# Kernel tuning notes

Hardware: AMD Instinct MI355X
Metric: run time of the kernel (lower is better)

Reference implementation:

```python
import jax, jax.numpy as jnp
import numpy as np

N = 100000      # nodes
E = 1000000     # edges (before self-loops)
IN_DIM = 256
H = 4           # heads
C = 32          # out_dim per head
NEG_SLOPE = 0.2  # PyG GATConv default negative_slope


def setup_inputs() -> dict:
    key = jax.random.key(0)
    ks = jax.random.split(key, 6)
    x = jax.random.normal(ks[0], (N, IN_DIM), jnp.float32)
    W = jax.random.normal(ks[1], (IN_DIM, H * C), jnp.float32) * (1.0 / np.sqrt(IN_DIM))
    a_src = jax.random.normal(ks[2], (H, C), jnp.float32) * 0.1
    a_dst = jax.random.normal(ks[3], (H, C), jnp.float32) * 0.1
    bias = jnp.zeros((H * C,), jnp.float32)
    edge_index = jax.random.randint(ks[4], (2, E), 0, N, dtype=jnp.int32)
    return {"x": x, "W": W, "a_src": a_src, "a_dst": a_dst, "bias": bias,
            "edge_index": edge_index}


def reference(x, W, a_src, a_dst, bias, edge_index):
    n = x.shape[0]
    # PyG GATConv default: add self-loops
    loops = jnp.arange(n, dtype=edge_index.dtype)
    src = jnp.concatenate([edge_index[0], loops])  # [E+N]
    dst = jnp.concatenate([edge_index[1], loops])  # [E+N]
    # linear transform -> [N, H, C]
    h = (x @ W).reshape(n, H, C)
    # per-node attention logits
    alpha_s = jnp.einsum('nhc,hc->nh', h, a_src)  # [N, H]
    alpha_d = jnp.einsum('nhc,hc->nh', h, a_dst)  # [N, H]
    # per-edge score, LeakyReLU
    e = jax.nn.leaky_relu(alpha_s[src] + alpha_d[dst], NEG_SLOPE)  # [E+N, H]
    # segment softmax over incoming edges of each destination node
    m = jax.lax.stop_gradient(jax.ops.segment_max(e, dst, num_segments=n))
    p = jnp.exp(e - m[dst])
    s = jax.ops.segment_sum(p, dst, num_segments=n)
    alpha = p / (s[dst] + 1e-16)  # [E+N, H]
    # weighted scatter-add of source features
    out = jax.ops.segment_sum(alpha[:, :, None] * h[src], dst, num_segments=n)  # [N, H, C]
    out = out.reshape(n, H * C) + bias
    return jnp.tanh(out)
```

## Files before the change

### kernel.cpp

```cpp
#include <hip/hip_runtime.h>

#define IN_DIM 256
#define HC     128
#define NHEAD  4
#define NEG    0.2f
#define CAP    256
#define AS     264
#define BKT    1024
#define NBMAX  128
#define EPT    16
#define BE     4096

typedef __attribute__((ext_vector_type(8))) short short8v;
typedef __attribute__((ext_vector_type(4))) float f32x4;
typedef __attribute__((ext_vector_type(4))) unsigned short ushort4v;

__device__ __forceinline__ unsigned short bf16_rn(float f) {
    unsigned u = __builtin_bit_cast(unsigned, f);
    return (unsigned short)((u + 0x7fffu + ((u >> 16) & 1u)) >> 16);
}
__device__ __forceinline__ float bf16_to_f32(unsigned short b) {
    unsigned u = ((unsigned)b) << 16;
    return __builtin_bit_cast(float, u);
}
__device__ __forceinline__ float fast_tanh(float x) {
    float t = __expf(2.f * x);
    return fmaf(-2.f, __builtin_amdgcn_rcpf(t + 1.f), 1.f);
}

__global__ void pack_w_kernel(const float* __restrict__ W,
                              unsigned short* __restrict__ w_hi) {
    int t = blockIdx.x * 256 + threadIdx.x;
    if (t >= 8 * 8 * 64) return;
    int l  = t & 63;
    int ct = (t >> 6) & 7;
    int s  = t >> 9;
    int kbase = s * 32 + (l >> 4) * 8;
    int col   = ct * 16 + (l & 15);
    size_t base = (size_t)t * 8;
#pragma unroll
    for (int e = 0; e < 8; ++e)
        w_hi[base + e] = bf16_rn(W[(size_t)(kbase + e) * HC + col]);
}

__global__ __launch_bounds__(512) void gemm_mfma_kernel(const float* __restrict__ x,
                                                        const unsigned short* __restrict__ w_hi,
                                                        const float* __restrict__ a_src,
                                                        const float* __restrict__ a_dst,
                                                        unsigned short* __restrict__ h_bf,
                                                        float* __restrict__ alpha_s,
                                                        float* __restrict__ alpha_d, int n) {
    __shared__ unsigned short s_hi[64][AS];
    __shared__ unsigned short s_lo[64][AS];
    __shared__ float pS[64][4];
    __shared__ float pD[64][4];

    const int tid = threadIdx.x;
    const int l   = tid & 63;
    const int wv  = tid >> 6;
    const int row0 = blockIdx.x * 64;

    const float4* x4 = reinterpret_cast<const float4*>(x);
#pragma unroll
    for (int i = 0; i < 8; ++i) {
        int f = tid + i * 512;
        int row = f >> 6, c4 = f & 63;
        float4 v = make_float4(0.f, 0.f, 0.f, 0.f);
        if (row0 + row < n) v = x4[(size_t)(row0 + row) * 64 + c4];
        float e[4] = {v.x, v.y, v.z, v.w};
        ushort4v hi, lo;
#pragma unroll
        for (int q = 0; q < 4; ++q) {
            unsigned short h16 = bf16_rn(e[q]);
            hi[q] = h16;
            lo[q] = bf16_rn(e[q] - bf16_to_f32(h16));
        }
        *reinterpret_cast<ushort4v*>(&s_hi[row][c4 * 4]) = hi;
        *reinterpret_cast<ushort4v*>(&s_lo[row][c4 * 4]) = lo;
    }
    __syncthreads();

    const int ct_g = wv & 3;
    const int rt_g = wv >> 2;
    const int rrow = l & 15;
    const int koff = (l >> 4) * 8;

    f32x4 acc[2][2];
#pragma unroll
    for (int a = 0; a < 2; ++a)
#pragma unroll
        for (int b = 0; b < 2; ++b) acc[a][b] = (f32x4){0.f, 0.f, 0.f, 0.f};

    for (int s = 0; s < 8; ++s) {
        short8v bh[2];
#pragma unroll
        for (int c = 0; c < 2; ++c) {
            int ct = ct_g * 2 + c;
            bh[c] = *reinterpret_cast<const short8v*>(w_hi + ((size_t)(s * 8 + ct) * 64 + l) * 8);
        }
#pragma unroll
        for (int r = 0; r < 2; ++r) {
            int arow = rt_g * 32 + r * 16 + rrow;
            short8v ah = *reinterpret_cast<const short8v*>(&s_hi[arow][koff + s * 32]);
            short8v al = *reinterpret_cast<const short8v*>(&s_lo[arow][koff + s * 32]);
#pragma unroll
            for (int c = 0; c < 2; ++c) {
                acc[r][c] = __builtin_amdgcn_mfma_f32_16x16x32_bf16(ah, bh[c], acc[r][c], 0, 0, 0);
                acc[r][c] = __builtin_amdgcn_mfma_f32_16x16x32_bf16(al, bh[c], acc[r][c], 0, 0, 0);
            }
        }
    }

#pragma unroll
    for (int r = 0; r < 2; ++r) {
#pragma unroll
        for (int c = 0; c < 2; ++c) {
            int col = (ct_g * 2 + c) * 16 + (l & 15);
#pragma unroll
            for (int q = 0; q < 4; ++q) {
                int row = row0 + rt_g * 32 + r * 16 + (l >> 4) * 4 + q;
                if (row < n) h_bf[(size_t)row * HC + col] = bf16_rn(acc[r][c][q]);
            }
        }
    }

    float asc[2], adc[2];
#pragma unroll
    for (int c = 0; c < 2; ++c) {
        int col = (ct_g * 2 + c) * 16 + (l & 15);
        asc[c] = a_src[col];
        adc[c] = a_dst[col];
    }
#pragma unroll
    for (int r = 0; r < 2; ++r) {
#pragma unroll
        for (int q = 0; q < 4; ++q) {
            float vS = acc[r][0][q] * asc[0] + acc[r][1][q] * asc[1];
            float vD = acc[r][0][q] * adc[0] + acc[r][1][q] * adc[1];
#pragma unroll
            for (int m = 1; m < 16; m <<= 1) {
                vS += __shfl_xor(vS, m);
                vD += __shfl_xor(vD, m);
            }
            if ((l & 15) == 0) {
                int rl = rt_g * 32 + r * 16 + (l >> 4) * 4 + q;
                pS[rl][ct_g] = vS;
                pD[rl][ct_g] = vD;
            }
        }
    }
    __syncthreads();
    if (tid < 256) {
        int rl = tid >> 2, h = tid & 3;
        int row = row0 + rl;
        if (row < n) {
            alpha_s[(size_t)row * 4 + h] = pS[rl][h];
            alpha_d[(size_t)row * 4 + h] = pD[rl][h];
        }
    }
}

__global__ __launch_bounds__(256) void bucket_hist_kernel(const int* __restrict__ ei,
                                                          int* __restrict__ bucket_cnt,
                                                          int E, int nb) {
    __shared__ int lh[NBMAX];
    int tid = threadIdx.x;
    if (tid < NBMAX) lh[tid] = 0;
    __syncthreads();
    int base = blockIdx.x * BE;
#pragma unroll
    for (int i = 0; i < EPT; ++i) {
        int e = base + i * 256 + tid;
        if (e < E) atomicAdd(&lh[ei[E + e] >> 10], 1);
    }
    __syncthreads();
    if (tid < nb && lh[tid]) atomicAdd(&bucket_cnt[tid], lh[tid]);
}

__global__ __launch_bounds__(128) void bucket_scan_kernel(const int* __restrict__ bucket_cnt,
                                                          int* __restrict__ bucket_base,
                                                          int* __restrict__ bucket_cursor,
                                                          int nb) {
    __shared__ int ws0[1];
    int t = threadIdx.x;
    int v = (t < nb) ? bucket_cnt[t] : 0;
    int lane = t & 63, wd = t >> 6;
    int x = v;
#pragma unroll
    for (int off = 1; off < 64; off <<= 1) {
        int y = __shfl_up(x, off);
        if (lane >= off) x += y;
    }
    if (wd == 0 && lane == 63) ws0[0] = x;
    __syncthreads();
    int wo = wd ? ws0[0] : 0;
    int excl = wo + x - v;
    if (t < nb) { bucket_base[t] = excl; bucket_cursor[t] = excl; }
    if (t == 127) bucket_base[nb] = wo + x;
}

__global__ __launch_bounds__(256) void bucket_scatter_kernel(const int* __restrict__ ei,
                                                             int* __restrict__ bucket_cursor,
                                                             unsigned* __restrict__ bucket_data,
                                                             int E, int nb) {
    __shared__ int lh[NBMAX];
    __shared__ int lofs[NBMAX];
    __shared__ int gofs[NBMAX];
    __shared__ int ws0[1];
    __shared__ unsigned buf[BE];

    int tid = threadIdx.x;
    if (tid < NBMAX) lh[tid] = 0;
    __syncthreads();

    int base = blockIdx.x * BE;
    int bb[EPT]; unsigned wv[EPT]; int rr[EPT];
#pragma unroll
    for (int i = 0; i < EPT; ++i) {
        int e = base + i * 256 + tid;
        if (e < E) {
            int src = ei[e];
            int dst = ei[E + e];
            bb[i] = dst >> 10;
            wv[i] = (unsigned)src | ((unsigned)(dst & 1023) << 17);
            rr[i] = atomicAdd(&lh[bb[i]], 1);
        } else bb[i] = -1;
    }
    __syncthreads();

    int v_ = 0, x_ = 0;
    int lane = tid & 63, wd = tid >> 6;
    if (tid < NBMAX) {
        v_ = lh[tid]; x_ = v_;
#pragma unroll
        for (int off = 1; off < 64; off <<= 1) {
            int y = __shfl_up(x_, off);
            if (lane >= off) x_ += y;
        }
        if (wd == 0 && lane == 63) ws0[0] = x_;
    }
    __syncthreads();
    if (tid < NBMAX) {
        int wo = wd ? ws0[0] : 0;
        lofs[tid] = wo + x_ - v_;
    }
    __syncthreads();

#pragma unroll
    for (int i = 0; i < EPT; ++i)
        if (bb[i] >= 0) buf[lofs[bb[i]] + rr[i]] = wv[i];
    if (tid < nb) gofs[tid] = lh[tid] ? atomicAdd(&bucket_cursor[tid], lh[tid]) : 0;
    __syncthreads();

    int wid = tid >> 6;
    for (int bk = wid; bk < nb; bk += 4) {
        int lo = lofs[bk], cnt = lh[bk], g = gofs[bk];
        for (int j = lane; j < cnt; j += 64)
            bucket_data[g + j] = buf[lo + j];
    }
}

__global__ __launch_bounds__(1024) void bucket_build_kernel(const int* __restrict__ bucket_base,
                                                            const unsigned* __restrict__ bucket_data,
                                                            int* __restrict__ deg,
                                                            int* __restrict__ row_start,
                                                            int* __restrict__ csr_src, int n) {
    __shared__ int lc[BKT];
    __shared__ int sc[BKT];
    __shared__ int wsum[16];

    int b = blockIdx.x;
    int base = bucket_base[b];
    int end  = bucket_base[b + 1];
    int t = threadIdx.x;

    lc[t] = 0;
    __syncthreads();
    for (int i = base + t; i < end; i += 1024)
        atomicAdd(&lc[bucket_data[i] >> 17], 1);
    __syncthreads();

    int val = lc[t];
    int lane = t & 63, wd = t >> 6;
    int x = val;
#pragma unroll
    for (int off = 1; off < 64; off <<= 1) {
        int y = __shfl_up(x, off);
        if (lane >= off) x += y;
    }
    if (lane == 63) wsum[wd] = x;
    __syncthreads();
    if (wd == 0 && lane < 16) {
        int y = wsum[lane];
#pragma unroll
        for (int off = 1; off < 16; off <<= 1) {
            int z = __shfl_up(y, off);
            if (lane >= off) y += z;
        }
        wsum[lane] = y;
    }
    __syncthreads();
    int wo = wd ? wsum[wd - 1] : 0;
    int excl = wo + x - val;
    sc[t] = excl;
    int v = b * BKT + t;
    if (v < n) { deg[v] = val; row_start[v] = base + excl; }
    lc[t] = 0;
    __syncthreads();

    for (int i = base + t; i < end; i += 1024) {
        unsigned w = bucket_data[i];
        int d = w >> 17;
        int src = (int)(w & 0x1FFFFu);
        int p = atomicAdd(&lc[d], 1);
        csr_src[base + sc[d] + p] = src;
    }
}

__global__ __launch_bounds__(256) void gather_kernel(const int* __restrict__ row_start,
                                                     const int* __restrict__ deg,
                                                     const int* __restrict__ csr_src,
                                                     const float* __restrict__ alpha_s,
                                                     const float* __restrict__ alpha_d,
                                                     const unsigned short* __restrict__ h_bf,
                                                     const float* __restrict__ bias,
                                                     float* __restrict__ out, int n) {
    __shared__ float wbuf[4][NHEAD][CAP + 4];
    __shared__ int   sbuf[4][CAP];
    int lane = threadIdx.x & 63;
    int wid  = threadIdx.x >> 6;
    int v = blockIdx.x * 4 + wid;
    if (v >= n) return;
    int start = row_start[v];
    int cnt = deg[v];
    int head = lane >> 4;
    int sub  = lane & 15;
    float* wp = wbuf[wid][head];
    int* sp = sbuf[wid];

    float adH = alpha_d[(size_t)v * 4 + head];

    float s = 0.f;
    for (int j = sub; j < cnt; j += 16) {
        int src = csr_src[start + j];
        float as = alpha_s[(size_t)src * 4 + head];
        float e = as + adH;
        e = e > 0.f ? e : NEG * e;
        float p = __expf(e);
        if (j < CAP) {
            wp[j] = p;
            if (head == 0) sp[j] = src;
        }
        s += p;
    }
#pragma unroll
    for (int off = 1; off < 16; off <<= 1) s += __shfl_xor(s, off);

    float asH = alpha_s[(size_t)v * 4 + head];
    float es = asH + adH;
    es = es > 0.f ? es : NEG * es;
    float pself = __expf(es);
    s += pself;
    float invH = __builtin_amdgcn_rcpf(s + 1e-16f);

    float accx = 0.f, accy = 0.f;
    const unsigned* hb = reinterpret_cast<const unsigned*>(h_bf);
    int m = cnt < CAP ? cnt : CAP;
    int j = 0;
    for (; j + 4 <= m; j += 4) {
        int4   s4 = *reinterpret_cast<const int4*>(&sp[j]);
        float4 w4 = *reinterpret_cast<const float4*>(&wp[j]);
        unsigned hA = hb[((unsigned)s4.x << 6) + lane];
        unsigned hB = hb[((unsigned)s4.y << 6) + lane];
        unsigned hC = hb[((unsigned)s4.z << 6) + lane];
        unsigned hD = hb[((unsigned)s4.w << 6) + lane];
        accx = fmaf(w4.x, bf16_to_f32((unsigned short)(hA & 0xffffu)), accx);
        accy = fmaf(w4.x, bf16_to_f32((unsigned short)(hA >> 16)),     accy);
        accx = fmaf(w4.y, bf16_to_f32((unsigned short)(hB & 0xffffu)), accx);
        accy = fmaf(w4.y, bf16_to_f32((unsigned short)(hB >> 16)),     accy);
        accx = fmaf(w4.z, bf16_to_f32((unsigned short)(hC & 0xffffu)), accx);
        accy = fmaf(w4.z, bf16_to_f32((unsigned short)(hC >> 16)),     accy);
        accx = fmaf(w4.w, bf16_to_f32((unsigned short)(hD & 0xffffu)), accx);
        accy = fmaf(w4.w, bf16_to_f32((unsigned short)(hD >> 16)),     accy);
    }
    for (; j < m; ++j) {
        int src = sp[j];
        float w = wp[j];
        unsigned hv = hb[((unsigned)src << 6) + lane];
        accx = fmaf(w, bf16_to_f32((unsigned short)(hv & 0xffffu)), accx);
        accy = fmaf(w, bf16_to_f32((unsigned short)(hv >> 16)),     accy);
    }
    for (; j < cnt; ++j) {
        int src = csr_src[start + j];
        float as = alpha_s[(size_t)src * 4 + head];
        float e = as + adH;
        e = e > 0.f ? e : NEG * e;
        float w = __expf(e);
        unsigned hv = hb[((unsigned)src << 6) + lane];
        accx = fmaf(w, bf16_to_f32((unsigned short)(hv & 0xffffu)), accx);
        accy = fmaf(w, bf16_to_f32((unsigned short)(hv >> 16)),     accy);
    }
    {
        unsigned hv = hb[((unsigned)v << 6) + lane];
        accx = fmaf(pself, bf16_to_f32((unsigned short)(hv & 0xffffu)), accx);
        accy = fmaf(pself, bf16_to_f32((unsigned short)(hv >> 16)),     accy);
    }
    float2 b = reinterpret_cast<const float2*>(bias)[lane];
    float2 o;
    o.x = fast_tanh(fmaf(accx, invH, b.x));
    o.y = fast_tanh(fmaf(accy, invH, b.y));
    reinterpret_cast<float2*>(out)[(size_t)v * 64 + lane] = o;
}

extern "C" void kernel_launch(void* const* d_in, const int* in_sizes, int n_in,
                              void* d_out, int out_size, void* d_ws, size_t ws_size,
                              hipStream_t stream) {
    const float* x     = (const float*)d_in[0];
    const float* W     = (const float*)d_in[1];
    const float* a_src = (const float*)d_in[2];
    const float* a_dst = (const float*)d_in[3];
    const float* bias  = (const float*)d_in[4];
    const int*   ei    = (const int*)d_in[5];

    const int n = in_sizes[0] / IN_DIM;
    const int E = in_sizes[5] / 2;
    const int nb = (n + BKT - 1) / BKT;

    float* ws = (float*)d_ws;
    size_t off = 0;
    unsigned short* h_bf = (unsigned short*)(ws + off); off += (size_t)n * HC / 2;
    float* alpha_s = ws + off; off += (size_t)n * NHEAD;
    float* alpha_d = ws + off; off += (size_t)n * NHEAD;
    unsigned short* w_hi = (unsigned short*)(ws + off); off += 16384;
    int* ibase        = (int*)(ws + off);
    int* deg          = ibase;
    int* row_start    = ibase + n;
    int* bucket_cnt   = ibase + 2 * (size_t)n;
    int* bucket_base  = bucket_cnt + NBMAX;
    int* bucket_cursor= bucket_base + NBMAX + 1;
    unsigned* bucket_data = (unsigned*)(bucket_cursor + NBMAX);
    int* csr_src      = (int*)(bucket_data + E);

    float* out = (float*)d_out;

    const int nblkE = (E + BE - 1) / BE;

    hipMemsetAsync(bucket_cnt, 0, NBMAX * sizeof(int), stream);

    pack_w_kernel<<<16, 256, 0, stream>>>(W, w_hi);
    gemm_mfma_kernel<<<(n + 63) / 64, 512, 0, stream>>>(x, w_hi, a_src, a_dst,
                                                        h_bf, alpha_s, alpha_d, n);

    bucket_hist_kernel<<<nblkE, 256, 0, stream>>>(ei, bucket_cnt, E, nb);
    bucket_scan_kernel<<<1, 128, 0, stream>>>(bucket_cnt, bucket_base, bucket_cursor, nb);
    bucket_scatter_kernel<<<nblkE, 256, 0, stream>>>(ei, bucket_cursor, bucket_data, E, nb);
    bucket_build_kernel<<<nb, 1024, 0, stream>>>(bucket_base, bucket_data,
                                                 deg, row_start, csr_src, n);

    gather_kernel<<<(n + 3) / 4, 256, 0, stream>>>(row_start, deg, csr_src,
                                                   alpha_s, alpha_d, h_bf, bias, out, n);
}
```

Measured before the change: 160.1 us.

## Fuse softmax-weight pass into single-pass gather with 8-way unrolled loads

The gather kernel drops its two-pass scheme, which first computed edge weights into LDS and then re-read them for accumulation. It now computes each edge's exp weight and accumulates both the denominator and the weighted bf16 features in one pass, unrolled by 8 to keep more independent loads in flight. This removes the LDS buffers and the extra pass, at the cost of every lane redundantly loading csr_src and alpha_s per edge. It also simplifies the bf16 unpacking and LeakyReLU arithmetic.

After: 153.3 us. -4.3%, faster.

```diff
diff --git a/kernel.cpp b/kernel.cpp
--- a/kernel.cpp
+++ b/kernel.cpp
@@ -4,7 +4,6 @@
 #define HC     128
 #define NHEAD  4
 #define NEG    0.2f
-#define CAP    256
 #define AS     264
 #define BKT    1024
 #define NBMAX  128
@@ -23,9 +22,18 @@
     unsigned u = ((unsigned)b) << 16;
     return __builtin_bit_cast(float, u);
 }
+__device__ __forceinline__ float bf16_lo(unsigned v) {
+    return __builtin_bit_cast(float, v << 16);
+}
+__device__ __forceinline__ float bf16_hi(unsigned v) {
+    return __builtin_bit_cast(float, v & 0xffff0000u);
+}
 __device__ __forceinline__ float fast_tanh(float x) {
     float t = __expf(2.f * x);
     return fmaf(-2.f, __builtin_amdgcn_rcpf(t + 1.f), 1.f);
+}
+__device__ __forceinline__ float lrelu(float e) {
+    return fmaxf(e, NEG * e);
 }
 
 __global__ void pack_w_kernel(const float* __restrict__ W,
@@ -325,8 +333,6 @@
                                                      const unsigned short* __restrict__ h_bf,
                                                      const float* __restrict__ bias,
                                                      float* __restrict__ out, int n) {
-    __shared__ float wbuf[4][NHEAD][CAP + 4];
-    __shared__ int   sbuf[4][CAP];
     int lane = threadIdx.x & 63;
     int wid  = threadIdx.x >> 6;
     int v = blockIdx.x * 4 + wid;
@@ -334,77 +340,95 @@
     int start = row_start[v];
     int cnt = deg[v];
     int head = lane >> 4;
-    int sub  = lane & 15;
-    float* wp = wbuf[wid][head];
-    int* sp = sbuf[wid];
+
+    const unsigned* hb = reinterpret_cast<const unsigned*>(h_bf);
 
     float adH = alpha_d[(size_t)v * 4 + head];
-
-    float s = 0.f;
-    for (int j = sub; j < cnt; j += 16) {
-        int src = csr_src[start + j];
-        float as = alpha_s[(size_t)src * 4 + head];
-        float e = as + adH;
-        e = e > 0.f ? e : NEG * e;
-        float p = __expf(e);
-        if (j < CAP) {
-            wp[j] = p;
-            if (head == 0) sp[j] = src;
-        }
-        s += p;
-    }
-#pragma unroll
-    for (int off = 1; off < 16; off <<= 1) s += __shfl_xor(s, off);
-
     float asH = alpha_s[(size_t)v * 4 + head];
-    float es = asH + adH;
-    es = es > 0.f ? es : NEG * es;
-    float pself = __expf(es);
-    s += pself;
+    float pself = __expf(lrelu(asH + adH));
+    unsigned hv0 = hb[((unsigned)v << 6) + lane];
+    float s = pself;
+    float accx = pself * bf16_lo(hv0);
+    float accy = pself * bf16_hi(hv0);
+
+    int j = 0;
+    for (; j + 8 <= cnt; j += 8) {
+        int s0 = csr_src[start + j + 0];
+        int s1 = csr_src[start + j + 1];
+        int s2 = csr_src[start + j + 2];
+        int s3 = csr_src[start + j + 3];
+        int s4 = csr_src[start + j + 4];
+        int s5 = csr_src[start + j + 5];
+        int s6 = csr_src[start + j + 6];
+        int s7 = csr_src[start + j + 7];
+        float a0 = alpha_s[(size_t)s0 * 4 + head];
+        float a1 = alpha_s[(size_t)s1 * 4 + head];
+        float a2 = alpha_s[(size_t)s2 * 4 + head];
+        float a3 = alpha_s[(size_t)s3 * 4 + head];
+        float a4 = alpha_s[(size_t)s4 * 4 + head];
+        float a5 = alpha_s[(size_t)s5 * 4 + head];
+        float a6 = alpha_s[(size_t)s6 * 4 + head];
+        float a7 = alpha_s[(size_t)s7 * 4 + head];
+        unsigned h0 = hb[((unsigned)s0 << 6) + lane];
+        unsigned h1 = hb[((unsigned)s1 << 6) + lane];
+        unsigned h2 = hb[((unsigned)s2 << 6) + lane];
+        unsigned h3 = hb[((unsigned)s3 << 6) + lane];
+        unsigned h4 = hb[((unsigned)s4 << 6) + lane];
+        unsigned h5 = hb[((unsigned)s5 << 6) + lane];
+        unsigned h6 = hb[((unsigned)s6 << 6) + lane];
+        unsigned h7 = hb[((unsigned)s7 << 6) + lane];
+        float w0 = __expf(lrelu(a0 + adH));
+        float w1 = __expf(lrelu(a1 + adH));
+        float w2 = __expf(lrelu(a2 + adH));
+        float w3 = __expf(lrelu(a3 + adH));
+        float w4 = __expf(lrelu(a4 + adH));
+        float w5 = __expf(lrelu(a5 + adH));
+        float w6 = __expf(lrelu(a6 + adH));
+        float w7 = __expf(lrelu(a7 + adH));
+        s += w0 + w1 + w2 + w3 + w4 + w5 + w6 + w7;
+        accx = fmaf(w0, bf16_lo(h0), accx); accy = fmaf(w0, bf16_hi(h0), accy);
+        accx = fmaf(w1, bf16_lo(h1), accx); accy = fmaf(w1, bf16_hi(h1), accy);
+        accx = fmaf(w2, bf16_lo(h2), accx); accy = fmaf(w2, bf16_hi(h2), accy);
+        accx = fmaf(w3, bf16_lo(h3), accx); accy = fmaf(w3, bf16_hi(h3), accy);
+        accx = fmaf(w4, bf16_lo(h4), accx); accy = fmaf(w4, bf16_hi(h4), accy);
+        accx = fmaf(w5, bf16_lo(h5), accx); accy = fmaf(w5, bf16_hi(h5), accy);
+        accx = fmaf(w6, bf16_lo(h6), accx); accy = fmaf(w6, bf16_hi(h6), accy);
+        accx = fmaf(w7, bf16_lo(h7), accx); accy = fmaf(w7, bf16_hi(h7), accy);
+    }
+    for (; j + 4 <= cnt; j += 4) {
+        int s0 = csr_src[start + j + 0];
+        int s1 = csr_src[start + j + 1];
+        int s2 = csr_src[start + j + 2];
+        int s3 = csr_src[start + j + 3];
+        float a0 = alpha_s[(size_t)s0 * 4 + head];
+        float a1 = alpha_s[(size_t)s1 * 4 + head];
+        float a2 = alpha_s[(size_t)s2 * 4 + head];
+        float a3 = alpha_s[(size_t)s3 * 4 + head];
+        unsigned h0 = hb[((unsigned)s0 << 6) + lane];
+        unsigned h1 = hb[((unsigned)s1 << 6) + lane];
+        unsigned h2 = hb[((unsigned)s2 << 6) + lane];
+        unsigned h3 = hb[((unsigned)s3 << 6) + lane];
+        float w0 = __expf(lrelu(a0 + adH));
+        float w1 = __expf(lrelu(a1 + adH));
+        float w2 = __expf(lrelu(a2 + adH));
+        float w3 = __expf(lrelu(a3 + adH));
+        s += w0 + w1 + w2 + w3;
+        accx = fmaf(w0, bf16_lo(h0), accx); accy = fmaf(w0, bf16_hi(h0), accy);
+        accx = fmaf(w1, bf16_lo(h1), accx); accy = fmaf(w1, bf16_hi(h1), accy);
+        accx = fmaf(w2, bf16_lo(h2), accx); accy = fmaf(w2, bf16_hi(h2), accy);
+        accx = fmaf(w3, bf16_lo(h3), accx); accy = fmaf(w3, bf16_hi(h3), accy);
+    }
+    for (; j < cnt; ++j) {
+        int s0 = csr_src[start + j];
+        float a0 = alpha_s[(size_t)s0 * 4 + head];
+        unsigned h0 = hb[((unsigned)s0 << 6) + lane];
+        float w0 = __expf(lrelu(a0 + adH));
+        s += w0;
+        accx = fmaf(w0, bf16_lo(h0), accx);
+        accy = fmaf(w0, bf16_hi(h0), accy);
+    }
+
     float invH = __builtin_amdgcn_rcpf(s + 1e-16f);
-
-    float accx = 0.f, accy = 0.f;
-    const unsigned* hb = reinterpret_cast<const unsigned*>(h_bf);
-    int m = cnt < CAP ? cnt : CAP;
-    int j = 0;
-    for (; j + 4 <= m; j += 4) {
-        int4   s4 = *reinterpret_cast<const int4*>(&sp[j]);
-        float4 w4 = *reinterpret_cast<const float4*>(&wp[j]);
-        unsigned hA = hb[((unsigned)s4.x << 6) + lane];
-        unsigned hB = hb[((unsigned)s4.y << 6) + lane];
-        unsigned hC = hb[((unsigned)s4.z << 6) + lane];
-        unsigned hD = hb[((unsigned)s4.w << 6) + lane];
-        accx = fmaf(w4.x, bf16_to_f32((unsigned short)(hA & 0xffffu)), accx);
-        accy = fmaf(w4.x, bf16_to_f32((unsigned short)(hA >> 16)),     accy);
-        accx = fmaf(w4.y, bf16_to_f32((unsigned short)(hB & 0xffffu)), accx);
-        accy = fmaf(w4.y, bf16_to_f32((unsigned short)(hB >> 16)),     accy);
-        accx = fmaf(w4.z, bf16_to_f32((unsigned short)(hC & 0xffffu)), accx);
-        accy = fmaf(w4.z, bf16_to_f32((unsigned short)(hC >> 16)),     accy);
-        accx = fmaf(w4.w, bf16_to_f32((unsigned short)(hD & 0xffffu)), accx);
-        accy = fmaf(w4.w, bf16_to_f32((unsigned short)(hD >> 16)),     accy);
-    }
-    for (; j < m; ++j) {
-        int src = sp[j];
-        float w = wp[j];
-        unsigned hv = hb[((unsigned)src << 6) + lane];
-        accx = fmaf(w, bf16_to_f32((unsigned short)(hv & 0xffffu)), accx);
-        accy = fmaf(w, bf16_to_f32((unsigned short)(hv >> 16)),     accy);
-    }
-    for (; j < cnt; ++j) {
-        int src = csr_src[start + j];
-        float as = alpha_s[(size_t)src * 4 + head];
-        float e = as + adH;
-        e = e > 0.f ? e : NEG * e;
-        float w = __expf(e);
-        unsigned hv = hb[((unsigned)src << 6) + lane];
-        accx = fmaf(w, bf16_to_f32((unsigned short)(hv & 0xffffu)), accx);
-        accy = fmaf(w, bf16_to_f32((unsigned short)(hv >> 16)),     accy);
-    }
-    {
-        unsigned hv = hb[((unsigned)v << 6) + lane];
-        accx = fmaf(pself, bf16_to_f32((unsigned short)(hv & 0xffffu)), accx);
-        accy = fmaf(pself, bf16_to_f32((unsigned short)(hv >> 16)),     accy);
-    }
     float2 b = reinterpret_cast<const float2*>(bias)[lane];
     float2 o;
     o.x = fast_tanh(fmaf(accx, invH, b.x));
```
